# Kernel tuning notes

Hardware: AMD Instinct MI355X
Metric: run time of the kernel (lower is better)

The kernel has to match this reference:

```python
import jax, jax.numpy as jnp
import numpy as np

DIM = 1024
HEADS = 16
HEAD_DIM = DIM // HEADS


def setup_inputs() -> dict:
    key = jax.random.key(0)
    ks = jax.random.split(key, 10)
    B, T, D = 4, 2048, DIM
    s = 1.0 / np.sqrt(D)
    inp = {
        "x": jax.random.normal(ks[0], (B, T, D), dtype=jnp.float32),
        "Wq": jax.random.normal(ks[1], (D, D), dtype=jnp.float32) * s,
        "bq": jnp.zeros((D,), dtype=jnp.float32),
        "Wk": jax.random.normal(ks[2], (D, D), dtype=jnp.float32) * s,
        "bk": jnp.zeros((D,), dtype=jnp.float32),
        "Wv": jax.random.normal(ks[3], (D, D), dtype=jnp.float32) * s,
        "bv": jnp.zeros((D,), dtype=jnp.float32),
        "Wo": jax.random.normal(ks[4], (D, D), dtype=jnp.float32) * s,
        "bo": jnp.zeros((D,), dtype=jnp.float32),
        "gamma": jnp.ones((D,), dtype=jnp.float32),
        "beta": jnp.zeros((D,), dtype=jnp.float32),
    }
    return inp


def _layernorm(x, gamma, beta, eps=1e-5):
    mu = jnp.mean(x, axis=-1, keepdims=True)
    var = jnp.var(x, axis=-1, keepdims=True)
    return (x - mu) * jax.lax.rsqrt(var + eps) * gamma + beta


def reference(x, Wq, bq, Wk, bk, Wv, bv, Wo, bo, gamma, beta):
    B, T, D = x.shape
    residual = x
    xn = _layernorm(x, gamma, beta)
    # torch Linear: x @ W.T + b ; reshape to [B, H, T, hd]
    def proj(W, b):
        return (xn @ W.T + b).reshape(B, T, HEADS, HEAD_DIM).transpose(0, 2, 1, 3)
    q = proj(Wq, bq)
    k = proj(Wk, bk)
    v = proj(Wv, bv)
    scores = jnp.einsum("bhqd,bhkd->bhqk", q, k) / np.sqrt(HEAD_DIM)
    causal = jnp.triu(jnp.ones((T, T), dtype=bool), k=1)  # True above diagonal
    scores = jnp.where(causal[None, None, :, :], jnp.float32(-1e9), scores)
    attn = jax.nn.softmax(scores, axis=-1)
    # dropout is identity in eval mode
    out = jnp.einsum("bhqk,bhkd->bhqd", attn, v)
    out = out.transpose(0, 2, 1, 3).reshape(B, T, D)
    return residual + out @ Wo.T + bo
```

## Files before the change

kernel.cpp:

```cpp
#include <hip/hip_runtime.h>
#include <hip/hip_bf16.h>
#include <stdint.h>

#define DIM   1024
#define TLEN  2048
#define HD    64
#define MROWS 8192

typedef __bf16 bf16x8 __attribute__((ext_vector_type(8)));
typedef float  f32x4  __attribute__((ext_vector_type(4)));

union PFrag { uint32_t w[4]; bf16x8 v; };

__device__ __forceinline__ uint32_t bf16rnd(float f){
  uint32_t u = __builtin_bit_cast(uint32_t, f);
  return (u + 0x7FFFu + ((u >> 16) & 1u)) >> 16;
}
__device__ __forceinline__ uint32_t pack2(float a, float b){
  return bf16rnd(a) | (bf16rnd(b) << 16);
}

#define GLDS(g, l) __builtin_amdgcn_global_load_lds( \
    (const __attribute__((address_space(1))) void*)(g), \
    (__attribute__((address_space(3))) void*)(l), 16, 0, 0)

__global__ __launch_bounds__(256) void cvt_kernel(
    const float* __restrict__ s0, const float* __restrict__ s1,
    const float* __restrict__ s2, const float* __restrict__ s3,
    uint16_t* __restrict__ d0, uint16_t* __restrict__ d1,
    uint16_t* __restrict__ d2, uint16_t* __restrict__ d3)
{
  const float* src; uint16_t* dst;
  if (blockIdx.y == 0){ src = s0; dst = d0; }
  else if (blockIdx.y == 1){ src = s1; dst = d1; }
  else if (blockIdx.y == 2){ src = s2; dst = d2; }
  else { src = s3; dst = d3; }
  const int i = blockIdx.x * 256 + threadIdx.x;
  const float4 f = *reinterpret_cast<const float4*>(src + (size_t)i * 4);
  uint32_t* d = reinterpret_cast<uint32_t*>(dst + (size_t)i * 4);
  d[0] = pack2(f.x, f.y);
  d[1] = pack2(f.z, f.w);
}

__global__ __launch_bounds__(256) void ln_kernel(
    const float* __restrict__ x, const float* __restrict__ gamma,
    const float* __restrict__ beta, uint16_t* __restrict__ xn)
{
  const int row = blockIdx.x;
  const int tid = threadIdx.x;
  const float4 v = *reinterpret_cast<const float4*>(x + (size_t)row * DIM + tid * 4);
  float s  = (v.x + v.y) + (v.z + v.w);
  float ss = (v.x * v.x + v.y * v.y) + (v.z * v.z + v.w * v.w);
#pragma unroll
  for (int off = 1; off < 64; off <<= 1){
    s  += __shfl_xor(s, off);
    ss += __shfl_xor(ss, off);
  }
  __shared__ float red[8];
  if ((tid & 63) == 0){ red[tid >> 6] = s; red[(tid >> 6) + 4] = ss; }
  __syncthreads();
  s  = (red[0] + red[1]) + (red[2] + red[3]);
  ss = (red[4] + red[5]) + (red[6] + red[7]);
  const float mu   = s * (1.0f / DIM);
  const float var  = ss * (1.0f / DIM) - mu * mu;
  const float rstd = rsqrtf(var + 1e-5f);
  const float4 g  = *reinterpret_cast<const float4*>(gamma + tid * 4);
  const float4 bt = *reinterpret_cast<const float4*>(beta  + tid * 4);
  const float o0 = (v.x - mu) * rstd * g.x + bt.x;
  const float o1 = (v.y - mu) * rstd * g.y + bt.y;
  const float o2 = (v.z - mu) * rstd * g.z + bt.z;
  const float o3 = (v.w - mu) * rstd * g.w + bt.w;
  uint32_t* dst = reinterpret_cast<uint32_t*>(xn + (size_t)row * DIM + tid * 4);
  dst[0] = pack2(o0, o1);
  dst[1] = pack2(o2, o3);
}

template<int EPI>
__device__ __forceinline__ void gemm_body(
    const uint16_t* __restrict__ A, const uint16_t* __restrict__ W,
    const float* __restrict__ bias,
    uint16_t* __restrict__ Cb, float* __restrict__ Cf,
    const float* __restrict__ res, float scale)
{
  __shared__ uint16_t As[128 * 32];
  __shared__ uint16_t Bs[128 * 32];
  const int tid  = threadIdx.x;
  const int lane = tid & 63;
  const int w    = tid >> 6;
  const int wr   = w >> 1, wc = w & 1;
  const int row0 = blockIdx.y * 128;
  const int col0 = blockIdx.x * 128;

  f32x4 acc[4][4] = {};

  const int srow = lane >> 2;
  const int scol = (lane & 3) * 8;
  const uint16_t* a0 = A + (size_t)(row0 + w * 32 + srow) * DIM + scol;
  const uint16_t* a1 = a0 + (size_t)16 * DIM;
  const uint16_t* b0 = W + (size_t)(col0 + w * 32 + srow) * DIM + scol;
  const uint16_t* b1 = b0 + (size_t)16 * DIM;
  uint16_t* la0 = &As[w * 1024];
  uint16_t* la1 = &As[w * 1024 + 512];
  uint16_t* lb0 = &Bs[w * 1024];
  uint16_t* lb1 = &Bs[w * 1024 + 512];

  const int fr = lane & 15, fg = lane >> 4;

  for (int k0 = 0; k0 < DIM; k0 += 32){
    GLDS(a0 + k0, la0);
    GLDS(a1 + k0, la1);
    GLDS(b0 + k0, lb0);
    GLDS(b1 + k0, lb1);
    __syncthreads();
    bf16x8 af[4], bfv[4];
#pragma unroll
    for (int m = 0; m < 4; ++m)
      af[m] = *reinterpret_cast<const bf16x8*>(&As[(wr * 64 + m * 16 + fr) * 32 + fg * 8]);
#pragma unroll
    for (int n = 0; n < 4; ++n)
      bfv[n] = *reinterpret_cast<const bf16x8*>(&Bs[(wc * 64 + n * 16 + fr) * 32 + fg * 8]);
#pragma unroll
    for (int m = 0; m < 4; ++m)
#pragma unroll
      for (int n = 0; n < 4; ++n)
        acc[m][n] = __builtin_amdgcn_mfma_f32_16x16x32_bf16(af[m], bfv[n], acc[m][n], 0, 0, 0);
    __syncthreads();
  }

#pragma unroll
  for (int m = 0; m < 4; ++m){
    const int rbase = row0 + wr * 64 + m * 16 + fg * 4;
#pragma unroll
    for (int n = 0; n < 4; ++n){
      const int c = col0 + wc * 64 + n * 16 + fr;
      const float bv = bias[c];
      if (EPI == 0){
#pragma unroll
        for (int r = 0; r < 4; ++r){
          float v = (acc[m][n][r] + bv) * scale;
          Cb[(size_t)(rbase + r) * DIM + c] = (uint16_t)bf16rnd(v);
        }
      } else {
#pragma unroll
        for (int r = 0; r < 4; ++r){
          size_t idx = (size_t)(rbase + r) * DIM + c;
          Cf[idx] = acc[m][n][r] + bv + res[idx];
        }
      }
    }
  }
}

__global__ __launch_bounds__(256) void qkv_gemm(
    const uint16_t* __restrict__ xn,
    const uint16_t* __restrict__ Wq, const uint16_t* __restrict__ Wk,
    const uint16_t* __restrict__ Wv,
    const float* __restrict__ bq, const float* __restrict__ bk,
    const float* __restrict__ bv,
    uint16_t* __restrict__ Qo, uint16_t* __restrict__ Ko, uint16_t* __restrict__ Vo)
{
  const uint16_t* W; const float* bias; uint16_t* out; float scale;
  if (blockIdx.z == 0){ W = Wq; bias = bq; out = Qo; scale = 0.125f; }
  else if (blockIdx.z == 1){ W = Wk; bias = bk; out = Ko; scale = 1.0f; }
  else { W = Wv; bias = bv; out = Vo; scale = 1.0f; }
  gemm_body<0>(xn, W, bias, out, nullptr, nullptr, scale);
}

__global__ __launch_bounds__(256) void out_gemm(
    const uint16_t* __restrict__ AO, const uint16_t* __restrict__ Wo,
    const float* __restrict__ bo, const float* __restrict__ res,
    float* __restrict__ out)
{
  gemm_body<1>(AO, Wo, bo, nullptr, out, res, 1.0f);
}

__global__ __launch_bounds__(256) void attn_kernel(
    const uint16_t* __restrict__ Q, const uint16_t* __restrict__ K,
    const uint16_t* __restrict__ V, uint16_t* __restrict__ O)
{
  __shared__ uint16_t Kl[64 * 72];
  __shared__ uint16_t Vt[64 * 72];
  const int tid  = threadIdx.x;
  const int lane = tid & 63;
  const int w    = tid >> 6;
  const int fr   = lane & 15, fg = lane >> 4;
  const int b = blockIdx.z, h = blockIdx.y, p = blockIdx.x;
  const int qtA = p, qtB = 31 - p;
  const size_t rowb = (size_t)b * TLEN;
  const int hoff = h * HD;

  const int qgA = qtA * 64 + w * 16 + fr;
  const int qgB = qtB * 64 + w * 16 + fr;

  const bf16x8 qA0 = *reinterpret_cast<const bf16x8*>(Q + (rowb + qgA) * DIM + hoff + fg * 8);
  const bf16x8 qA1 = *reinterpret_cast<const bf16x8*>(Q + (rowb + qgA) * DIM + hoff + 32 + fg * 8);
  const bf16x8 qB0 = *reinterpret_cast<const bf16x8*>(Q + (rowb + qgB) * DIM + hoff + fg * 8);
  const bf16x8 qB1 = *reinterpret_cast<const bf16x8*>(Q + (rowb + qgB) * DIM + hoff + 32 + fg * 8);

  f32x4 oA[4] = {}, oB[4] = {};
  float mA = -1e30f, lA = 0.0f, mB = -1e30f, lB = 0.0f;

  const int kr = tid >> 2, kc = (tid & 3) * 16;
  const int vd = tid & 63, vq = tid >> 6;
  const int vf = ((vd >> 3) & 7) << 3;

  for (int kt = 0; kt <= qtB; ++kt){
    const int kv0 = kt * 64;
    {
      const uint16_t* ksrc = K + (rowb + kv0 + kr) * DIM + hoff + kc;
      *reinterpret_cast<bf16x8*>(&Kl[kr * 72 + kc])     = *reinterpret_cast<const bf16x8*>(ksrc);
      *reinterpret_cast<bf16x8*>(&Kl[kr * 72 + kc + 8]) = *reinterpret_cast<const bf16x8*>(ksrc + 8);
      const uint16_t* vsrc = V + (rowb + kv0 + vq * 16) * DIM + hoff + vd;
#pragma unroll
      for (int kk = 0; kk < 16; ++kk)
        Vt[vd * 72 + ((vq * 16 + kk) ^ vf)] = vsrc[(size_t)kk * DIM];
    }
    __syncthreads();

    auto step = [&](const bf16x8& q0, const bf16x8& q1, f32x4 (&oacc)[4],
                    float& mr, float& lr, const int qg, const bool diag){
      f32x4 s[4];
#pragma unroll
      for (int t = 0; t < 4; ++t){
        const bf16x8 kf0 = *reinterpret_cast<const bf16x8*>(&Kl[(t * 16 + fr) * 72 + fg * 8]);
        const bf16x8 kf1 = *reinterpret_cast<const bf16x8*>(&Kl[(t * 16 + fr) * 72 + 32 + fg * 8]);
        f32x4 z = {};
        z = __builtin_amdgcn_mfma_f32_16x16x32_bf16(kf0, q0, z, 0, 0, 0);
        z = __builtin_amdgcn_mfma_f32_16x16x32_bf16(kf1, q1, z, 0, 0, 0);
        s[t] = z;
      }

      float mloc = -1e30f;
      if (diag){
#pragma unroll
        for (int t = 0; t < 4; ++t)
#pragma unroll
          for (int r = 0; r < 4; ++r){
            const int kvg = kv0 + t * 16 + fg * 4 + r;
            const float sv = (kvg <= qg) ? s[t][r] : -1e30f;
            s[t][r] = sv;
            mloc = fmaxf(mloc, sv);
          }
      } else {
#pragma unroll
        for (int t = 0; t < 4; ++t)
#pragma unroll
          for (int r = 0; r < 4; ++r) mloc = fmaxf(mloc, s[t][r]);
      }
      mloc = fmaxf(mloc, __shfl_xor(mloc, 16));
      mloc = fmaxf(mloc, __shfl_xor(mloc, 32));
      const float mnew  = fmaxf(mr, mloc);
      const float alpha = __expf(mr - mnew);
      mr = mnew;

      uint32_t plo[4], phi[4];
      float psum = 0.0f;
#pragma unroll
      for (int t = 0; t < 4; ++t){
        const float p0 = __expf(s[t][0] - mnew);
        const float p1 = __expf(s[t][1] - mnew);
        const float p2 = __expf(s[t][2] - mnew);
        const float p3 = __expf(s[t][3] - mnew);
        psum += (p0 + p1) + (p2 + p3);
        plo[t] = pack2(p0, p1);
        phi[t] = pack2(p2, p3);
      }
      psum += __shfl_xor(psum, 16);
      psum += __shfl_xor(psum, 32);
      lr = lr * alpha + psum;
#pragma unroll
      for (int dt = 0; dt < 4; ++dt) oacc[dt] *= alpha;

      const int  src0 = fr + ((lane >> 4) & 1) * 32;
      const bool hi   = lane >= 32;
#pragma unroll
      for (int kb = 0; kb < 2; ++kb){
        const uint32_t la  = (uint32_t)__shfl((int)plo[2 * kb],     src0);
        const uint32_t lb  = (uint32_t)__shfl((int)plo[2 * kb + 1], src0);
        const uint32_t ha  = (uint32_t)__shfl((int)phi[2 * kb],     src0);
        const uint32_t hb  = (uint32_t)__shfl((int)phi[2 * kb + 1], src0);
        const uint32_t la2 = (uint32_t)__shfl((int)plo[2 * kb],     src0 + 16);
        const uint32_t lb2 = (uint32_t)__shfl((int)plo[2 * kb + 1], src0 + 16);
        const uint32_t ha2 = (uint32_t)__shfl((int)phi[2 * kb],     src0 + 16);
        const uint32_t hb2 = (uint32_t)__shfl((int)phi[2 * kb + 1], src0 + 16);
        PFrag pf;
        pf.w[0] = hi ? lb  : la;
        pf.w[1] = hi ? hb  : ha;
        pf.w[2] = hi ? lb2 : la2;
        pf.w[3] = hi ? hb2 : ha2;
#pragma unroll
        for (int dt = 0; dt < 4; ++dt){
          const int d = dt * 16 + fr;
          const int f = ((d >> 3) & 7) << 3;
          const bf16x8 vfr = *reinterpret_cast<const bf16x8*>(
              &Vt[d * 72 + ((kb * 32 + fg * 8) ^ f)]);
          oacc[dt] = __builtin_amdgcn_mfma_f32_16x16x32_bf16(vfr, pf.v, oacc[dt], 0, 0, 0);
        }
      }
    };

    if (kt <= qtA) step(qA0, qA1, oA, mA, lA, qgA, kt == qtA);
    step(qB0, qB1, oB, mB, lB, qgB, kt == qtB);
    __syncthreads();
  }

  const float invA = 1.0f / lA;
  const float invB = 1.0f / lB;
#pragma unroll
  for (int dt = 0; dt < 4; ++dt){
    uint32_t* dstA = reinterpret_cast<uint32_t*>(
        O + (rowb + qgA) * DIM + hoff + dt * 16 + fg * 4);
    dstA[0] = pack2(oA[dt][0] * invA, oA[dt][1] * invA);
    dstA[1] = pack2(oA[dt][2] * invA, oA[dt][3] * invA);
    uint32_t* dstB = reinterpret_cast<uint32_t*>(
        O + (rowb + qgB) * DIM + hoff + dt * 16 + fg * 4);
    dstB[0] = pack2(oB[dt][0] * invB, oB[dt][1] * invB);
    dstB[1] = pack2(oB[dt][2] * invB, oB[dt][3] * invB);
  }
}

extern "C" void kernel_launch(void* const* d_in, const int* in_sizes, int n_in,
                              void* d_out, int out_size, void* d_ws, size_t ws_size,
                              hipStream_t stream) {
  const float* x     = (const float*)d_in[0];
  const float* Wq    = (const float*)d_in[1];
  const float* bq    = (const float*)d_in[2];
  const float* Wk    = (const float*)d_in[3];
  const float* bk    = (const float*)d_in[4];
  const float* Wv    = (const float*)d_in[5];
  const float* bv    = (const float*)d_in[6];
  const float* Wo    = (const float*)d_in[7];
  const float* bo    = (const float*)d_in[8];
  const float* gamma = (const float*)d_in[9];
  const float* beta  = (const float*)d_in[10];
  float* out = (float*)d_out;

  uint8_t* ws = (uint8_t*)d_ws;
  uint16_t* xn  = (uint16_t*)(ws);
  uint16_t* Wqb = (uint16_t*)(ws + 16777216);
  uint16_t* Wkb = (uint16_t*)(ws + 16777216 + 1 * 2097152);
  uint16_t* Wvb = (uint16_t*)(ws + 16777216 + 2 * 2097152);
  uint16_t* Wob = (uint16_t*)(ws + 16777216 + 3 * 2097152);
  uint16_t* Qb  = (uint16_t*)(ws + 25165824);
  uint16_t* Kb  = (uint16_t*)(ws + 25165824 + 1 * 16777216);
  uint16_t* Vb  = (uint16_t*)(ws + 25165824 + 2 * 16777216);
  uint16_t* AOb = (uint16_t*)(ws + 25165824 + 3 * 16777216);

  cvt_kernel<<<dim3(1024, 4), 256, 0, stream>>>(Wq, Wk, Wv, Wo, Wqb, Wkb, Wvb, Wob);
  ln_kernel<<<8192, 256, 0, stream>>>(x, gamma, beta, xn);
  qkv_gemm<<<dim3(8, 64, 3), 256, 0, stream>>>(xn, Wqb, Wkb, Wvb, bq, bk, bv, Qb, Kb, Vb);
  attn_kernel<<<dim3(16, 16, 4), 256, 0, stream>>>(Qb, Kb, Vb, AOb);
  out_gemm<<<dim3(8, 64, 1), 256, 0, stream>>>(AOb, Wob, bo, x, out);
}
```

Measured before the change: 334.7 us.

## Prefetch next K/V tile into registers and use lazy softmax rescaling

The attention loop now loads the next K/V tile from global memory into registers while the current tile is being computed, then writes it to LDS at the start of the next iteration. This hides global-load latency behind MFMA work. The V transpose store is packed into 32-bit LDS writes. Online softmax rescaling is done only when the running max grows by more than a threshold of 8, which skips most exp and multiply work but lets unnormalised exponents reach up to e^8. Prefetching costs extra registers, which may lower occupancy.

```diff
diff --git a/kernel.cpp b/kernel.cpp
--- a/kernel.cpp
+++ b/kernel.cpp
@@ -204,18 +204,38 @@
   const int vd = tid & 63, vq = tid >> 6;
   const int vf = ((vd >> 3) & 7) << 3;
 
+  const uint16_t* kbase = K + (rowb + kr) * DIM + hoff + kc;
+  const uint16_t* vbase = V + (rowb + vq * 16) * DIM + hoff + vd;
+
+  bf16x8 kst0, kst1;
+  uint16_t vst[16];
+
+  auto load_tile = [&](int kt, bf16x8& k0, bf16x8& k1, uint16_t (&vr)[16]){
+    const size_t koff = (size_t)kt * 64 * DIM;
+    k0 = *reinterpret_cast<const bf16x8*>(kbase + koff);
+    k1 = *reinterpret_cast<const bf16x8*>(kbase + koff + 8);
+    const uint16_t* vsrc = vbase + koff;
+#pragma unroll
+    for (int kk = 0; kk < 16; ++kk)
+      vr[kk] = vsrc[(size_t)kk * DIM];
+  };
+
+  load_tile(0, kst0, kst1, vst);
+
   for (int kt = 0; kt <= qtB; ++kt){
     const int kv0 = kt * 64;
-    {
-      const uint16_t* ksrc = K + (rowb + kv0 + kr) * DIM + hoff + kc;
-      *reinterpret_cast<bf16x8*>(&Kl[kr * 72 + kc])     = *reinterpret_cast<const bf16x8*>(ksrc);
-      *reinterpret_cast<bf16x8*>(&Kl[kr * 72 + kc + 8]) = *reinterpret_cast<const bf16x8*>(ksrc + 8);
-      const uint16_t* vsrc = V + (rowb + kv0 + vq * 16) * DIM + hoff + vd;
-#pragma unroll
-      for (int kk = 0; kk < 16; ++kk)
-        Vt[vd * 72 + ((vq * 16 + kk) ^ vf)] = vsrc[(size_t)kk * DIM];
+    *reinterpret_cast<bf16x8*>(&Kl[kr * 72 + kc])     = kst0;
+    *reinterpret_cast<bf16x8*>(&Kl[kr * 72 + kc + 8]) = kst1;
+#pragma unroll
+    for (int j = 0; j < 8; ++j){
+      const uint32_t word = (uint32_t)vst[2 * j] | ((uint32_t)vst[2 * j + 1] << 16);
+      *reinterpret_cast<uint32_t*>(&Vt[vd * 72 + ((vq * 16 + 2 * j) ^ vf)]) = word;
     }
     __syncthreads();
+
+    bf16x8 nk0, nk1;
+    uint16_t nv[16];
+    if (kt < qtB) load_tile(kt + 1, nk0, nk1, nv);
 
     auto step = [&](const bf16x8& q0, const bf16x8& q1, f32x4 (&oacc)[4],
                     float& mr, float& lr, const int qg, const bool diag){
@@ -249,27 +269,30 @@
       }
       mloc = fmaxf(mloc, __shfl_xor(mloc, 16));
       mloc = fmaxf(mloc, __shfl_xor(mloc, 32));
-      const float mnew  = fmaxf(mr, mloc);
-      const float alpha = __expf(mr - mnew);
-      mr = mnew;
+
+      if (mloc > mr + 8.0f){
+        const float alpha = __expf(mr - mloc);
+        mr = mloc;
+        lr *= alpha;
+#pragma unroll
+        for (int dt = 0; dt < 4; ++dt) oacc[dt] *= alpha;
+      }
 
       uint32_t plo[4], phi[4];
       float psum = 0.0f;
 #pragma unroll
       for (int t = 0; t < 4; ++t){
-        const float p0 = __expf(s[t][0] - mnew);
-        const float p1 = __expf(s[t][1] - mnew);
-        const float p2 = __expf(s[t][2] - mnew);
-        const float p3 = __expf(s[t][3] - mnew);
+        const float p0 = __expf(s[t][0] - mr);
+        const float p1 = __expf(s[t][1] - mr);
+        const float p2 = __expf(s[t][2] - mr);
+        const float p3 = __expf(s[t][3] - mr);
         psum += (p0 + p1) + (p2 + p3);
         plo[t] = pack2(p0, p1);
         phi[t] = pack2(p2, p3);
       }
       psum += __shfl_xor(psum, 16);
       psum += __shfl_xor(psum, 32);
-      lr = lr * alpha + psum;
-#pragma unroll
-      for (int dt = 0; dt < 4; ++dt) oacc[dt] *= alpha;
+      lr += psum;
 
       const int  src0 = fr + ((lane >> 4) & 1) * 32;
       const bool hi   = lane >= 32;
@@ -302,6 +325,12 @@
     if (kt <= qtA) step(qA0, qA1, oA, mA, lA, qgA, kt == qtA);
     step(qB0, qB1, oB, mB, lB, qgB, kt == qtB);
     __syncthreads();
+
+    if (kt < qtB){
+      kst0 = nk0; kst1 = nk1;
+#pragma unroll
+      for (int kk = 0; kk < 16; ++kk) vst[kk] = nv[kk];
+    }
   }
 
   const float invA = 1.0f / lA;
```

Measured after the change: 335.4 us. Within noise of the previous version (+0.2%).
